# Kernel tuning notes

Measured on AMD Instinct MI355X. Metric: run time of the kernel, lower is better.

## Reference

```python
import math
import jax, jax.numpy as jnp
import numpy as np

V_NODES = 100000
N_EDGES = 1600000
EMBED = 768
HID = 256
H = 4
FH = HID // H
L = 2
PE_D = EMBED // 4  # 192
SLOPE = 0.2


def make_pe(max_len, d):
    pos = np.arange(max_len, dtype=np.float32)[:, None]
    div = np.exp(np.arange(0, d, 2, dtype=np.float32) * (-math.log(10000.0) / d))
    pe = np.zeros((max_len, d), dtype=np.float32)
    pe[:, 0::2] = np.sin(pos * div)
    pe[:, 1::2] = np.cos(pos * div)
    return jnp.asarray(pe)


def setup_inputs() -> dict:
    key = jax.random.key(0)
    ks = jax.random.split(key, 24)

    def xavier(k, shape):
        fan_in, fan_out = shape[0], shape[1]
        lim = math.sqrt(6.0 / (fan_in + fan_out))
        return jax.random.uniform(k, shape, jnp.float32, -lim, lim)

    in_proj_dim = EMBED + 2 * PE_D  # 1152
    inp = {
        'row_idx': jax.random.randint(ks[0], (V_NODES,), 0, 256),
        'col_idx': jax.random.randint(ks[1], (V_NODES,), 0, 64),
        'edge_index': jax.random.randint(ks[2], (2, N_EDGES), 0, V_NODES),
        'edge_weight': jax.random.uniform(ks[3], (N_EDGES,), jnp.float32),
        'W_in': xavier(ks[4], (in_proj_dim, HID)),
        'b_in': jnp.zeros((HID,), jnp.float32),
        'ln_g': jnp.ones((HID,), jnp.float32),
        'ln_b': jnp.zeros((HID,), jnp.float32),
        'Wq': jnp.stack([xavier(ks[5 + i], (HID, HID)) for i in range(L)]),
        'bq': jnp.zeros((L, HID), jnp.float32),
        'Wk': jnp.stack([xavier(ks[7 + i], (HID, HID)) for i in range(L)]),
        'bk': jnp.zeros((L, HID), jnp.float32),
        'Wv': jnp.stack([xavier(ks[9 + i], (HID, HID)) for i in range(L)]),
        'bv': jnp.zeros((L, HID), jnp.float32),
        'Wo': jnp.stack([xavier(ks[11 + i], (HID, HID)) for i in range(L)]),
        'bo': jnp.zeros((L, HID), jnp.float32),
        'We': jnp.stack([xavier(ks[13 + i], (1, H)) for i in range(L)]),  # edge_proj weight [1,H]
        'be': jnp.zeros((L, H), jnp.float32),
    }
    return inp


def gat_layer(h, src, tgt, ew, Wq, bq, Wk, bk, Wv, bv, Wo, bo, We, be):
    V = h.shape[0]
    Q = (h @ Wq + bq).reshape(V, H, FH)
    K = (h @ Wk + bk).reshape(V, H, FH)
    Vo = (h @ Wv + bv).reshape(V, H, FH)
    # edge bias: Linear(1,H) on edge_weight, then leaky relu -> [E,H]
    edge_bias = jax.nn.leaky_relu(ew[:, None] * We.reshape(1, H) + be, SLOPE)
    attn_raw = jnp.sum(Q[src] * K[tgt], axis=-1) / math.sqrt(FH) + edge_bias  # [E,H]
    attn_exp = jnp.exp(attn_raw)
    deg = jax.ops.segment_sum(attn_exp, tgt, num_segments=V) + 1e-16  # [V,H]
    attn_norm = attn_exp / deg[tgt]  # [E,H] (dropout is identity at eval)
    msg = Vo[src] * attn_norm[:, :, None] * ew[:, None, None]  # [E,H,FH]
    out = jax.ops.segment_sum(msg, tgt, num_segments=V).reshape(V, H * FH)
    return jax.nn.leaky_relu(out @ Wo + bo, SLOPE)


def reference(row_idx, col_idx, edge_index, edge_weight,
              W_in, b_in, ln_g, ln_b,
              Wq, bq, Wk, bk, Wv, bv, Wo, bo, We, be):
    V = row_idx.shape[0]
    row_pe = make_pe(256, PE_D)
    col_pe = make_pe(64, PE_D)
    cell = jnp.zeros((V, EMBED), jnp.float32)  # cell_embeds are zeros in source
    h = jnp.concatenate([cell, row_pe[row_idx], col_pe[col_idx]], axis=-1)
    # input_proj: Linear -> LayerNorm -> ReLU (dropout identity)
    h = h @ W_in + b_in
    mu = jnp.mean(h, axis=-1, keepdims=True)
    var = jnp.var(h, axis=-1, keepdims=True)
    h = (h - mu) / jnp.sqrt(var + 1e-5) * ln_g + ln_b
    h = jax.nn.relu(h)
    src, tgt = edge_index[0], edge_index[1]
    for i in range(L):
        h = gat_layer(h, src, tgt, edge_weight,
                      Wq[i], bq[i], Wk[i], bk[i], Wv[i], bv[i],
                      Wo[i], bo[i], We[i], be[i])
    return h
```

## Files before the change

kernel.cpp:

```cpp
#include <hip/hip_runtime.h>
#include <hip/hip_bf16.h>
#include <type_traits>
#include <math.h>

typedef __attribute__((ext_vector_type(8))) short bf16x8;
typedef __attribute__((ext_vector_type(4))) float f32x4;

__device__ __forceinline__ float bf2f(unsigned int u16) {
    union { unsigned int i; float f; } x; x.i = (u16 & 0xffffu) << 16; return x.f;
}
__device__ __forceinline__ unsigned int f2bf(float f) {
    union { float f; unsigned int i; } x; x.f = f;
    unsigned int i = x.i;
    unsigned int r = i + 0x7fffu + ((i >> 16) & 1u);
    return r >> 16;
}

#define SLOPE 0.2f

__global__ void k_hist(const int* __restrict__ tgt, int* __restrict__ cnt, int E) {
    int i = blockIdx.x * blockDim.x + threadIdx.x;
    if (i < E) atomicAdd(&cnt[tgt[i]], 1);
}

__global__ void __launch_bounds__(1024) k_scan1(const int* __restrict__ in, int* __restrict__ out,
                                                int* __restrict__ bsums, int n) {
    __shared__ int sm[1024];
    int i = blockIdx.x * 1024 + threadIdx.x;
    int v = (i < n) ? in[i] : 0;
    sm[threadIdx.x] = v; __syncthreads();
    for (int ofs = 1; ofs < 1024; ofs <<= 1) {
        int t = (threadIdx.x >= ofs) ? sm[threadIdx.x - ofs] : 0;
        __syncthreads();
        sm[threadIdx.x] += t;
        __syncthreads();
    }
    if (i < n) out[i] = sm[threadIdx.x];
    if (threadIdx.x == 1023) bsums[blockIdx.x] = sm[1023];
}

__global__ void __launch_bounds__(1024) k_scan2(int* bsums, int nb) {
    __shared__ int sm[1024];
    int v = (threadIdx.x < nb) ? bsums[threadIdx.x] : 0;
    sm[threadIdx.x] = v; __syncthreads();
    for (int ofs = 1; ofs < 1024; ofs <<= 1) {
        int t = (threadIdx.x >= ofs) ? sm[threadIdx.x - ofs] : 0;
        __syncthreads();
        sm[threadIdx.x] += t;
        __syncthreads();
    }
    if (threadIdx.x < nb) bsums[threadIdx.x] = sm[threadIdx.x] - v;
}

__global__ void __launch_bounds__(1024) k_scan3(int* __restrict__ out1, const int* __restrict__ bsums,
                                                int* __restrict__ off0, int n) {
    int i = blockIdx.x * 1024 + threadIdx.x;
    if (i < n) out1[i] += bsums[blockIdx.x];
    if (i == 0) off0[0] = 0;
}

__global__ void k_scatter(const int* __restrict__ ei, const float* __restrict__ ew,
                          const int* __restrict__ off, int* __restrict__ fill,
                          int* __restrict__ ssrc, float* __restrict__ sew, int E) {
    int e = blockIdx.x * blockDim.x + threadIdx.x;
    if (e < E) {
        int s = ei[e], t = ei[E + e];
        int pos = off[t] + atomicAdd(&fill[t], 1);
        ssrc[pos] = s; sew[pos] = ew[e];
    }
}

__global__ void k_combo(const int* __restrict__ ri, const int* __restrict__ ci,
                        int* __restrict__ combo, int V) {
    int v = blockIdx.x * blockDim.x + threadIdx.x;
    if (v < V) combo[v] = ri[v] * 64 + ci[v];
}

__global__ void __launch_bounds__(256) k_wt(const float* __restrict__ Wq, const float* __restrict__ Wk,
                                            const float* __restrict__ Wv, const float* __restrict__ Wo,
                                            unsigned short* __restrict__ WT) {
    __shared__ float sm[64][65];
    int blk = blockIdx.x;
    int m = blk >> 4, t = blk & 15;
    int tr = t >> 2, tc = t & 3;
    const float* srcs[4] = {Wq, Wk, Wv, Wo};
    const float* W = srcs[m & 3] + (size_t)(m >> 2) * 65536;
    int tid = threadIdx.x;
    for (int i = tid; i < 4096; i += 256) {
        int r = i >> 6, c = i & 63;
        sm[r][c] = W[(size_t)(tr * 64 + r) * 256 + tc * 64 + c];
    }
    __syncthreads();
    for (int i = tid; i < 4096; i += 256) {
        int n = i >> 6, k = i & 63;
        WT[(size_t)(m * 256 + tc * 64 + n) * 256 + tr * 64 + k] = (unsigned short)f2bf(sm[k][n]);
    }
}

__global__ void __launch_bounds__(256) k_bias(const float* __restrict__ bq, const float* __restrict__ bk,
                                              const float* __restrict__ bv, const float* __restrict__ bo,
                                              float* __restrict__ biasF) {
    int m = blockIdx.x, n = threadIdx.x;
    const float* srcs[4] = {bq, bk, bv, bo};
    biasF[m * 256 + n] = srcs[m & 3][(m >> 2) * 256 + n];
}

__global__ void __launch_bounds__(256) k_peproj(const float* __restrict__ W_in, float* __restrict__ AB) {
    __shared__ float pe[192];
    int blk = blockIdx.x;
    bool isA = blk < 256;
    int pos = isA ? blk : blk - 256;
    const float* Wb = W_in + (size_t)(isA ? 768 : 960) * 256;
    int tid = threadIdx.x;
    if (tid < 192) {
        float div = expf(-(float)(tid & ~1) * (logf(10000.0f) / 192.0f));
        float ang = (float)pos * div;
        pe[tid] = (tid & 1) ? cosf(ang) : sinf(ang);
    }
    __syncthreads();
    float acc = 0.f;
    #pragma unroll 8
    for (int d = 0; d < 192; ++d) acc = fmaf(pe[d], Wb[d * 256 + tid], acc);
    AB[blk * 256 + tid] = acc;
}

__global__ void __launch_bounds__(256) k_h0(const float* __restrict__ AB, const float* __restrict__ b_in,
                                            const float* __restrict__ g, const float* __restrict__ b,
                                            unsigned short* __restrict__ h0t) {
    int wid = threadIdx.x >> 6, lane = threadIdx.x & 63;
    int m = blockIdx.x * 4 + wid;
    int r = m >> 6, c = m & 63;
    float4 a  = ((const float4*)(AB + (size_t)r * 256))[lane];
    float4 bb = ((const float4*)(AB + (size_t)(256 + c) * 256))[lane];
    float4 bi = ((const float4*)b_in)[lane];
    float x0 = a.x + bb.x + bi.x, x1 = a.y + bb.y + bi.y;
    float x2 = a.z + bb.z + bi.z, x3 = a.w + bb.w + bi.w;
    float s = x0 + x1 + x2 + x3;
    #pragma unroll
    for (int msk = 1; msk < 64; msk <<= 1) s += __shfl_xor(s, msk);
    float mu = s * (1.f / 256.f);
    float d0 = x0 - mu, d1 = x1 - mu, d2 = x2 - mu, d3 = x3 - mu;
    float sq = d0 * d0 + d1 * d1 + d2 * d2 + d3 * d3;
    #pragma unroll
    for (int msk = 1; msk < 64; msk <<= 1) sq += __shfl_xor(sq, msk);
    float rstd = rsqrtf(sq * (1.f / 256.f) + 1e-5f);
    float4 gv = ((const float4*)g)[lane], bv = ((const float4*)b)[lane];
    float y0 = fmaxf(fmaf(d0 * rstd, gv.x, bv.x), 0.f);
    float y1 = fmaxf(fmaf(d1 * rstd, gv.y, bv.y), 0.f);
    float y2 = fmaxf(fmaf(d2 * rstd, gv.z, bv.z), 0.f);
    float y3 = fmaxf(fmaf(d3 * rstd, gv.w, bv.w), 0.f);
    uint2 o;
    o.x = f2bf(y0) | (f2bf(y1) << 16);
    o.y = f2bf(y2) | (f2bf(y3) << 16);
    *(uint2*)(h0t + (size_t)m * 256 + lane * 4) = o;
}

template <typename TC, bool LEAKY>
__global__ void __launch_bounds__(256) k_mm(const unsigned short* __restrict__ A,
                                            const unsigned short* __restrict__ WT,
                                            const float* __restrict__ bias,
                                            TC* __restrict__ C, int M, int ldc) {
    __shared__ __align__(16) unsigned short As[128][72];
    __shared__ __align__(16) unsigned short Bs[128][72];
    int tid = threadIdx.x;
    int R0 = blockIdx.x * 128, C0 = blockIdx.y * 128;
    int lane = tid & 63, wave = tid >> 6;
    int wr = (wave >> 1) * 64, wc = (wave & 1) * 64;
    int fr = lane & 15, fq = lane >> 4;
    f32x4 acc[4][4] = {};
    for (int k0 = 0; k0 < 256; k0 += 64) {
        for (int i = tid; i < 1024; i += 256) {
            int r = i >> 3, c8 = (i & 7) * 8;
            int gr = R0 + r;
            uint4 u = make_uint4(0u, 0u, 0u, 0u);
            if (gr < M) u = *(const uint4*)(A + (size_t)gr * 256 + k0 + c8);
            *(uint4*)&As[r][c8] = u;
            *(uint4*)&Bs[r][c8] = *(const uint4*)(WT + (size_t)(C0 + r) * 256 + k0 + c8);
        }
        __syncthreads();
        #pragma unroll
        for (int ks = 0; ks < 64; ks += 32) {
            bf16x8 af[4], bfv[4];
            #pragma unroll
            for (int mi = 0; mi < 4; ++mi) af[mi] = *(const bf16x8*)&As[wr + mi * 16 + fr][ks + fq * 8];
            #pragma unroll
            for (int ni = 0; ni < 4; ++ni) bfv[ni] = *(const bf16x8*)&Bs[wc + ni * 16 + fr][ks + fq * 8];
            #pragma unroll
            for (int mi = 0; mi < 4; ++mi)
                #pragma unroll
                for (int ni = 0; ni < 4; ++ni)
                    acc[mi][ni] = __builtin_amdgcn_mfma_f32_16x16x32_bf16(af[mi], bfv[ni], acc[mi][ni], 0, 0, 0);
        }
        __syncthreads();
    }
    #pragma unroll
    for (int mi = 0; mi < 4; ++mi) {
        #pragma unroll
        for (int r = 0; r < 4; ++r) {
            int row = R0 + wr + mi * 16 + fq * 4 + r;
            if (row >= M) continue;
            #pragma unroll
            for (int ni = 0; ni < 4; ++ni) {
                int col = C0 + wc + ni * 16 + fr;
                float v = acc[mi][ni][r] + bias[col];
                if (LEAKY) v = v > 0.f ? v : SLOPE * v;
                if constexpr (std::is_same<TC, float>::value) {
                    C[(size_t)row * ldc + col] = v;
                } else {
                    C[(size_t)row * ldc + col] = (unsigned short)f2bf(v);
                }
            }
        }
    }
}

template <bool USE_COMBO>
__global__ void __launch_bounds__(256) k_edge(const int* __restrict__ off, const int* __restrict__ ssrc,
                                              const float* __restrict__ sew, const int* __restrict__ combo,
                                              const unsigned short* __restrict__ QKV,
                                              const float* __restrict__ We_l, const float* __restrict__ be_l,
                                              unsigned short* __restrict__ out, int V) {
    int wid = threadIdx.x >> 6, lane = threadIdx.x & 63;
    int t = blockIdx.x * 4 + wid;
    if (t >= V) return;
    int h = lane >> 4;
    int krow = USE_COMBO ? combo[t] : t;
    uint2 ku = *(const uint2*)(QKV + (size_t)krow * 768 + 256 + lane * 4);
    float k0 = bf2f(ku.x), k1 = bf2f(ku.x >> 16), k2 = bf2f(ku.y), k3 = bf2f(ku.y >> 16);
    float Weh = We_l[h], beh = be_l[h];
    float n0 = 0.f, n1 = 0.f, n2 = 0.f, n3 = 0.f, den = 0.f;
    int beg = off[t], end = off[t + 1];
    for (int e0 = beg; e0 < end; e0 += 64) {
        int nrem = end - e0; if (nrem > 64) nrem = 64;
        int sv = 0; float wv = 0.f;
        if (lane < nrem) {
            sv = ssrc[e0 + lane];
            wv = sew[e0 + lane];
            if (USE_COMBO) sv = combo[sv];
        }
        for (int i = 0; i < nrem; ++i) {
            int srow = __shfl(sv, i);
            float w = __shfl(wv, i);
            uint2 qu = *(const uint2*)(QKV + (size_t)srow * 768 + lane * 4);
            float p = bf2f(qu.x) * k0 + bf2f(qu.x >> 16) * k1 + bf2f(qu.y) * k2 + bf2f(qu.y >> 16) * k3;
            p += __shfl_xor(p, 1);
            p += __shfl_xor(p, 2);
            p += __shfl_xor(p, 4);
            p += __shfl_xor(p, 8);
            float bias = fmaf(w, Weh, beh);
            bias = bias > 0.f ? bias : SLOPE * bias;
            float ex = expf(fmaf(p, 0.125f, bias));
            den += ex;
            float cc = ex * w;
            uint2 vu = *(const uint2*)(QKV + (size_t)srow * 768 + 512 + lane * 4);
            n0 = fmaf(cc, bf2f(vu.x), n0);
            n1 = fmaf(cc, bf2f(vu.x >> 16), n1);
            n2 = fmaf(cc, bf2f(vu.y), n2);
            n3 = fmaf(cc, bf2f(vu.y >> 16), n3);
        }
    }
    float inv = 1.f / (den + 1e-16f);
    uint2 o;
    o.x = f2bf(n0 * inv) | (f2bf(n1 * inv) << 16);
    o.y = f2bf(n2 * inv) | (f2bf(n3 * inv) << 16);
    *(uint2*)(out + (size_t)t * 256 + lane * 4) = o;
}

extern "C" void kernel_launch(void* const* d_in, const int* in_sizes, int n_in,
                              void* d_out, int out_size, void* d_ws, size_t ws_size,
                              hipStream_t stream) {
    const int*   row_idx = (const int*)d_in[0];
    const int*   col_idx = (const int*)d_in[1];
    const int*   ei      = (const int*)d_in[2];
    const float* ew      = (const float*)d_in[3];
    const float* W_in    = (const float*)d_in[4];
    const float* b_in    = (const float*)d_in[5];
    const float* ln_g    = (const float*)d_in[6];
    const float* ln_b    = (const float*)d_in[7];
    const float* Wq      = (const float*)d_in[8];
    const float* bq      = (const float*)d_in[9];
    const float* Wk      = (const float*)d_in[10];
    const float* bk      = (const float*)d_in[11];
    const float* Wv      = (const float*)d_in[12];
    const float* bv      = (const float*)d_in[13];
    const float* Wo      = (const float*)d_in[14];
    const float* bo      = (const float*)d_in[15];
    const float* We      = (const float*)d_in[16];
    const float* be      = (const float*)d_in[17];

    const int V = in_sizes[0];
    const int E = in_sizes[3];
    const int NC = 16384;

    char* w = (char*)d_ws;
    size_t o = 0;
    auto alloc = [&](size_t bytes) -> char* {
        char* p = w + o;
        o = (o + bytes + 255) & ~(size_t)255;
        return p;
    };
    int*   cnt     = (int*)alloc((size_t)V * 4);
    int*   fill    = (int*)alloc((size_t)V * 4);
    int*   csr_off = (int*)alloc((size_t)(V + 1) * 4);
    int*   bsums   = (int*)alloc(1024 * 4);
    int*   csr_src = (int*)alloc((size_t)E * 4);
    float* csr_ew  = (float*)alloc((size_t)E * 4);
    int*   combo   = (int*)alloc((size_t)V * 4);
    float* AB      = (float*)alloc((size_t)320 * 256 * 4);
    unsigned short* WT    = (unsigned short*)alloc((size_t)2048 * 256 * 2);
    float*          biasF = (float*)alloc((size_t)2048 * 4);
    unsigned short* h0t   = (unsigned short*)alloc((size_t)NC * 256 * 2);
    unsigned short* QKV1  = (unsigned short*)alloc((size_t)NC * 768 * 2);
    unsigned short* out_e = (unsigned short*)alloc((size_t)V * 256 * 2);
    unsigned short* h1    = (unsigned short*)alloc((size_t)V * 256 * 2);
    unsigned short* QKV2  = (unsigned short*)alloc((size_t)V * 768 * 2);

    hipMemsetAsync(cnt, 0, (size_t)V * 4, stream);
    hipMemsetAsync(fill, 0, (size_t)V * 4, stream);

    int eb = (E + 255) / 256;
    int nscan = (V + 1023) / 1024;
    k_hist<<<eb, 256, 0, stream>>>(ei + E, cnt, E);
    k_scan1<<<nscan, 1024, 0, stream>>>(cnt, csr_off + 1, bsums, V);
    k_scan2<<<1, 1024, 0, stream>>>(bsums, nscan);
    k_scan3<<<nscan, 1024, 0, stream>>>(csr_off + 1, bsums, csr_off, V);
    k_scatter<<<eb, 256, 0, stream>>>(ei, ew, csr_off, fill, csr_src, csr_ew, E);
    k_combo<<<(V + 255) / 256, 256, 0, stream>>>(row_idx, col_idx, combo, V);

    k_wt<<<128, 256, 0, stream>>>(Wq, Wk, Wv, Wo, WT);
    k_bias<<<8, 256, 0, stream>>>(bq, bk, bv, bo, biasF);
    k_peproj<<<320, 256, 0, stream>>>(W_in, AB);
    k_h0<<<NC / 4, 256, 0, stream>>>(AB, b_in, ln_g, ln_b, h0t);

    dim3 g1(NC / 128, 6);
    k_mm<unsigned short, false><<<g1, 256, 0, stream>>>(h0t, WT, biasF, QKV1, NC, 768);

    int tb = (V + 3) / 4;
    k_edge<true><<<tb, 256, 0, stream>>>(csr_off, csr_src, csr_ew, combo, QKV1, We, be, out_e, V);

    int mb = (V + 127) / 128;
    dim3 gо(mb, 2);
    dim3 gqkv(mb, 6);
    k_mm<unsigned short, true><<<gо, 256, 0, stream>>>(out_e, WT + (size_t)768 * 256, biasF + 768, h1, V, 256);
    k_mm<unsigned short, false><<<gqkv, 256, 0, stream>>>(h1, WT + (size_t)1024 * 256, biasF + 1024, QKV2, V, 768);

    k_edge<false><<<tb, 256, 0, stream>>>(csr_off, csr_src, csr_ew, combo, QKV2, We + 4, be + 4, out_e, V);

    k_mm<float, true><<<gо, 256, 0, stream>>>(out_e, WT + (size_t)1792 * 256, biasF + 1792, (float*)d_out, V, 256);
}
```

Baseline: 874.3 us.

## Restructure GEMM with full-K LDS tiles and direct loads; widen edge-gather vectors

The matmul kernel now loads a 128-row A tile covering the whole K=256 into LDS once, using global_load_lds with an XOR swizzle. It then loops over all N tiles in a single 512-thread block, so A is no longer re-fetched for each output column tile. The edge kernel splits each wave into two halves that process two edges at once with 16-byte loads, uses fast __expf, and combines the halves at the end. The trade-offs are 128KB of LDS per block, which limits occupancy to one block per CU, and a serialized N loop with a sync after each tile.

```diff
diff --git a/kernel.cpp b/kernel.cpp
--- a/kernel.cpp
+++ b/kernel.cpp
@@ -5,6 +5,9 @@
 
 typedef __attribute__((ext_vector_type(8))) short bf16x8;
 typedef __attribute__((ext_vector_type(4))) float f32x4;
+
+typedef __attribute__((address_space(3))) char       lds_char;
+typedef const __attribute__((address_space(1))) char g_char;
 
 __device__ __forceinline__ float bf2f(unsigned int u16) {
     union { unsigned int i; float f; } x; x.i = (u16 & 0xffffu) << 16; return x.f;
@@ -155,62 +158,87 @@
     *(uint2*)(h0t + (size_t)m * 256 + lane * 4) = o;
 }
 
-template <typename TC, bool LEAKY>
-__global__ void __launch_bounds__(256) k_mm(const unsigned short* __restrict__ A,
-                                            const unsigned short* __restrict__ WT,
-                                            const float* __restrict__ bias,
-                                            TC* __restrict__ C, int M, int ldc) {
-    __shared__ __align__(16) unsigned short As[128][72];
-    __shared__ __align__(16) unsigned short Bs[128][72];
+template <typename TC, bool LEAKY, int NT>
+__global__ void __launch_bounds__(512, 1) k_mm2(const unsigned short* __restrict__ A,
+                                                const unsigned short* __restrict__ WT,
+                                                const float* __restrict__ bias,
+                                                TC* __restrict__ C, int M, int ldc) {
+    __shared__ __align__(16) char AsB[65536];
+    __shared__ __align__(16) char BsB[65536];
     int tid = threadIdx.x;
-    int R0 = blockIdx.x * 128, C0 = blockIdx.y * 128;
     int lane = tid & 63, wave = tid >> 6;
-    int wr = (wave >> 1) * 64, wc = (wave & 1) * 64;
+    int R0 = blockIdx.x * 128;
+    int wr = (wave >> 2) * 64, wc = (wave & 3) * 32;
     int fr = lane & 15, fq = lane >> 4;
-    f32x4 acc[4][4] = {};
-    for (int k0 = 0; k0 < 256; k0 += 64) {
-        for (int i = tid; i < 1024; i += 256) {
-            int r = i >> 3, c8 = (i & 7) * 8;
-            int gr = R0 + r;
-            uint4 u = make_uint4(0u, 0u, 0u, 0u);
-            if (gr < M) u = *(const uint4*)(A + (size_t)gr * 256 + k0 + c8);
-            *(uint4*)&As[r][c8] = u;
-            *(uint4*)&Bs[r][c8] = *(const uint4*)(WT + (size_t)(C0 + r) * 256 + k0 + c8);
-        }
-        __syncthreads();
+
+    #pragma unroll
+    for (int it = 0; it < 8; ++it) {
+        int chunk = it * 512 + wave * 64 + lane;
+        int r = chunk >> 5, cb = (chunk & 31) * 16;
+        int sc = cb ^ ((r & 7) << 4);
+        int gr = R0 + r;
+        if (gr < M)
+            __builtin_amdgcn_global_load_lds(
+                (g_char*)((const char*)(A + (size_t)gr * 256) + sc),
+                (lds_char*)(AsB + (size_t)(it * 512 + wave * 64) * 16), 16, 0, 0);
+    }
+
+    for (int nt = 0; nt < NT; ++nt) {
         #pragma unroll
-        for (int ks = 0; ks < 64; ks += 32) {
-            bf16x8 af[4], bfv[4];
+        for (int it = 0; it < 8; ++it) {
+            int chunk = it * 512 + wave * 64 + lane;
+            int r = chunk >> 5, cb = (chunk & 31) * 16;
+            int sc = cb ^ ((r & 7) << 4);
+            __builtin_amdgcn_global_load_lds(
+                (g_char*)((const char*)(WT + (size_t)(nt * 128 + r) * 256) + sc),
+                (lds_char*)(BsB + (size_t)(it * 512 + wave * 64) * 16), 16, 0, 0);
+        }
+        __syncthreads();
+
+        f32x4 acc[4][2] = {};
+        #pragma unroll
+        for (int ks = 0; ks < 8; ++ks) {
+            int kb = ks * 64 + fq * 16;
+            bf16x8 af[4], bf[2];
             #pragma unroll
-            for (int mi = 0; mi < 4; ++mi) af[mi] = *(const bf16x8*)&As[wr + mi * 16 + fr][ks + fq * 8];
+            for (int mi = 0; mi < 4; ++mi) {
+                int r = wr + mi * 16 + fr;
+                af[mi] = *(const bf16x8*)(AsB + r * 512 + (kb ^ ((r & 7) << 4)));
+            }
             #pragma unroll
-            for (int ni = 0; ni < 4; ++ni) bfv[ni] = *(const bf16x8*)&Bs[wc + ni * 16 + fr][ks + fq * 8];
+            for (int ni = 0; ni < 2; ++ni) {
+                int r = wc + ni * 16 + fr;
+                bf[ni] = *(const bf16x8*)(BsB + r * 512 + (kb ^ ((r & 7) << 4)));
+            }
             #pragma unroll
             for (int mi = 0; mi < 4; ++mi)
                 #pragma unroll
-                for (int ni = 0; ni < 4; ++ni)
-                    acc[mi][ni] = __builtin_amdgcn_mfma_f32_16x16x32_bf16(af[mi], bfv[ni], acc[mi][ni], 0, 0, 0);
-        }
-        __syncthreads();
-    }
-    #pragma unroll
-    for (int mi = 0; mi < 4; ++mi) {
+                for (int ni = 0; ni < 2; ++ni)
+                    acc[mi][ni] = __builtin_amdgcn_mfma_f32_16x16x32_bf16(af[mi], bf[ni], acc[mi][ni], 0, 0, 0);
+        }
+
+        int C0 = nt * 128;
         #pragma unroll
-        for (int r = 0; r < 4; ++r) {
-            int row = R0 + wr + mi * 16 + fq * 4 + r;
-            if (row >= M) continue;
+        for (int mi = 0; mi < 4; ++mi) {
             #pragma unroll
-            for (int ni = 0; ni < 4; ++ni) {
-                int col = C0 + wc + ni * 16 + fr;
-                float v = acc[mi][ni][r] + bias[col];
-                if (LEAKY) v = v > 0.f ? v : SLOPE * v;
-                if constexpr (std::is_same<TC, float>::value) {
-                    C[(size_t)row * ldc + col] = v;
-                } else {
-                    C[(size_t)row * ldc + col] = (unsigned short)f2bf(v);
+            for (int r4 = 0; r4 < 4; ++r4) {
+                int row = R0 + wr + mi * 16 + fq * 4 + r4;
+                if (row < M) {
+                    #pragma unroll
+                    for (int ni = 0; ni < 2; ++ni) {
+                        int col = C0 + wc + ni * 16 + fr;
+                        float v = acc[mi][ni][r4] + bias[col];
+                        if (LEAKY) v = fmaxf(v, SLOPE * v);
+                        if constexpr (std::is_same<TC, float>::value) {
+                            C[(size_t)row * ldc + col] = v;
+                        } else {
+                            C[(size_t)row * ldc + col] = (unsigned short)f2bf(v);
+                        }
+                    }
                 }
             }
         }
+        __syncthreads();
     }
 }
 
@@ -223,12 +251,16 @@
     int wid = threadIdx.x >> 6, lane = threadIdx.x & 63;
     int t = blockIdx.x * 4 + wid;
     if (t >= V) return;
-    int h = lane >> 4;
+    int q = lane & 31, half = lane >> 5;
+    int h = q >> 3;
     int krow = USE_COMBO ? combo[t] : t;
-    uint2 ku = *(const uint2*)(QKV + (size_t)krow * 768 + 256 + lane * 4);
-    float k0 = bf2f(ku.x), k1 = bf2f(ku.x >> 16), k2 = bf2f(ku.y), k3 = bf2f(ku.y >> 16);
+    uint4 ku = *(const uint4*)(QKV + (size_t)krow * 768 + 256 + q * 8);
+    float kf[8];
+    kf[0] = bf2f(ku.x); kf[1] = bf2f(ku.x >> 16); kf[2] = bf2f(ku.y); kf[3] = bf2f(ku.y >> 16);
+    kf[4] = bf2f(ku.z); kf[5] = bf2f(ku.z >> 16); kf[6] = bf2f(ku.w); kf[7] = bf2f(ku.w >> 16);
     float Weh = We_l[h], beh = be_l[h];
-    float n0 = 0.f, n1 = 0.f, n2 = 0.f, n3 = 0.f, den = 0.f;
+    float n[8] = {0.f, 0.f, 0.f, 0.f, 0.f, 0.f, 0.f, 0.f};
+    float den = 0.f;
     int beg = off[t], end = off[t + 1];
     for (int e0 = beg; e0 < end; e0 += 64) {
         int nrem = end - e0; if (nrem > 64) nrem = 64;
@@ -238,32 +270,52 @@
             wv = sew[e0 + lane];
             if (USE_COMBO) sv = combo[sv];
         }
-        for (int i = 0; i < nrem; ++i) {
-            int srow = __shfl(sv, i);
-            float w = __shfl(wv, i);
-            uint2 qu = *(const uint2*)(QKV + (size_t)srow * 768 + lane * 4);
-            float p = bf2f(qu.x) * k0 + bf2f(qu.x >> 16) * k1 + bf2f(qu.y) * k2 + bf2f(qu.y >> 16) * k3;
+        for (int i = 0; i < nrem; i += 2) {
+            int ei = i + half;
+            int srow = __shfl(sv, ei);
+            float w  = __shfl(wv, ei);
+            const unsigned short* base = QKV + (size_t)srow * 768 + q * 8;
+            uint4 qu = *(const uint4*)base;
+            uint4 vu = *(const uint4*)(base + 512);
+            float p;
+            p = bf2f(qu.x) * kf[0];
+            p = fmaf(bf2f(qu.x >> 16), kf[1], p);
+            p = fmaf(bf2f(qu.y),       kf[2], p);
+            p = fmaf(bf2f(qu.y >> 16), kf[3], p);
+            p = fmaf(bf2f(qu.z),       kf[4], p);
+            p = fmaf(bf2f(qu.z >> 16), kf[5], p);
+            p = fmaf(bf2f(qu.w),       kf[6], p);
+            p = fmaf(bf2f(qu.w >> 16), kf[7], p);
             p += __shfl_xor(p, 1);
             p += __shfl_xor(p, 2);
             p += __shfl_xor(p, 4);
-            p += __shfl_xor(p, 8);
             float bias = fmaf(w, Weh, beh);
-            bias = bias > 0.f ? bias : SLOPE * bias;
-            float ex = expf(fmaf(p, 0.125f, bias));
+            bias = fmaxf(bias, SLOPE * bias);
+            float ex = (ei < nrem) ? __expf(fmaf(p, 0.125f, bias)) : 0.f;
             den += ex;
             float cc = ex * w;
-            uint2 vu = *(const uint2*)(QKV + (size_t)srow * 768 + 512 + lane * 4);
-            n0 = fmaf(cc, bf2f(vu.x), n0);
-            n1 = fmaf(cc, bf2f(vu.x >> 16), n1);
-            n2 = fmaf(cc, bf2f(vu.y), n2);
-            n3 = fmaf(cc, bf2f(vu.y >> 16), n3);
-        }
-    }
+            n[0] = fmaf(cc, bf2f(vu.x),       n[0]);
+            n[1] = fmaf(cc, bf2f(vu.x >> 16), n[1]);
+            n[2] = fmaf(cc, bf2f(vu.y),       n[2]);
+            n[3] = fmaf(cc, bf2f(vu.y >> 16), n[3]);
+            n[4] = fmaf(cc, bf2f(vu.z),       n[4]);
+            n[5] = fmaf(cc, bf2f(vu.z >> 16), n[5]);
+            n[6] = fmaf(cc, bf2f(vu.w),       n[6]);
+            n[7] = fmaf(cc, bf2f(vu.w >> 16), n[7]);
+        }
+    }
+    den += __shfl_xor(den, 32);
+    #pragma unroll
+    for (int j = 0; j < 8; ++j) n[j] += __shfl_xor(n[j], 32);
     float inv = 1.f / (den + 1e-16f);
-    uint2 o;
-    o.x = f2bf(n0 * inv) | (f2bf(n1 * inv) << 16);
-    o.y = f2bf(n2 * inv) | (f2bf(n3 * inv) << 16);
-    *(uint2*)(out + (size_t)t * 256 + lane * 4) = o;
+    if (half == 0) {
+        uint4 o;
+        o.x = f2bf(n[0] * inv) | (f2bf(n[1] * inv) << 16);
+        o.y = f2bf(n[2] * inv) | (f2bf(n[3] * inv) << 16);
+        o.z = f2bf(n[4] * inv) | (f2bf(n[5] * inv) << 16);
+        o.w = f2bf(n[6] * inv) | (f2bf(n[7] * inv) << 16);
+        *(uint4*)(out + (size_t)t * 256 + q * 8) = o;
+    }
 }
 
 extern "C" void kernel_launch(void* const* d_in, const int* in_sizes, int n_in,
@@ -332,19 +384,16 @@
     k_peproj<<<320, 256, 0, stream>>>(W_in, AB);
     k_h0<<<NC / 4, 256, 0, stream>>>(AB, b_in, ln_g, ln_b, h0t);
 
-    dim3 g1(NC / 128, 6);
-    k_mm<unsigned short, false><<<g1, 256, 0, stream>>>(h0t, WT, biasF, QKV1, NC, 768);
+    k_mm2<unsigned short, false, 6><<<NC / 128, 512, 0, stream>>>(h0t, WT, biasF, QKV1, NC, 768);
 
     int tb = (V + 3) / 4;
     k_edge<true><<<tb, 256, 0, stream>>>(csr_off, csr_src, csr_ew, combo, QKV1, We, be, out_e, V);
 
     int mb = (V + 127) / 128;
-    dim3 gо(mb, 2);
-    dim3 gqkv(mb, 6);
-    k_mm<unsigned short, true><<<gо, 256, 0, stream>>>(out_e, WT + (size_t)768 * 256, biasF + 768, h1, V, 256);
-    k_mm<unsigned short, false><<<gqkv, 256, 0, stream>>>(h1, WT + (size_t)1024 * 256, biasF + 1024, QKV2, V, 768);
+    k_mm2<unsigned short, true, 2><<<mb, 512, 0, stream>>>(out_e, WT + (size_t)768 * 256, biasF + 768, h1, V, 256);
+    k_mm2<unsigned short, false, 6><<<mb, 512, 0, stream>>>(h1, WT + (size_t)1024 * 256, biasF + 1024, QKV2, V, 768);
 
     k_edge<false><<<tb, 256, 0, stream>>>(csr_off, csr_src, csr_ew, combo, QKV2, We + 4, be + 4, out_e, V);
 
-    k_mm<float, true><<<gо, 256, 0, stream>>>(out_e, WT + (size_t)1792 * 256, biasF + 1792, (float*)d_out, V, 256);
-}
+    k_mm2<float, true, 2><<<mb, 512, 0, stream>>>(out_e, WT + (size_t)1792 * 256, biasF + 1792, (float*)d_out, V, 256);
+}
```

After: 917.0 us. +4.9%, slower.
